# Performance work log

Measured on AMD Instinct MI355X. Metric: run time of the kernel, lower is better.

Reference implementation:

```python
import jax, jax.numpy as jnp
import numpy as np

B = 64          # batches
T = 65536       # total packed tokens
X = 512         # token feature dim
K = 5           # io pairs
Y = X * K       # extra dim = 2560
H = 512         # hidden


def setup_inputs() -> dict:
    key = jax.random.key(0)
    ks = jax.random.split(key, 13)
    s = 0.02  # weight scale
    return {
        "ps_data": jax.random.normal(ks[0], (T, X), jnp.float32),
        "io_embed": jax.random.normal(ks[1], (B, K, X), jnp.float32),
        "segment_ids": jnp.sort(jax.random.randint(ks[2], (T,), 0, B, dtype=jnp.int32)),
        # attention_fc: Linear(X+Y,512) -> ReLU -> Linear(512,512) -> ReLU -> Linear(512,1)
        "W1": jax.random.normal(ks[3], (X + Y, H), jnp.float32) * s,
        "b1": jnp.zeros((H,), jnp.float32),
        "W2": jax.random.normal(ks[4], (H, H), jnp.float32) * s,
        "b2": jnp.zeros((H,), jnp.float32),
        "W3": jax.random.normal(ks[5], (H, 1), jnp.float32) * s,
        "b3": jnp.zeros((1,), jnp.float32),
        # final_fc: Linear(512,512) -> ReLU -> Linear(512,2)
        "Wf1": jax.random.normal(ks[6], (H, H), jnp.float32) * s,
        "bf1": jnp.zeros((H,), jnp.float32),
        "Wf2": jax.random.normal(ks[7], (H, 2), jnp.float32) * s,
        "bf2": jnp.zeros((2,), jnp.float32),
    }


def reference(ps_data, io_embed, segment_ids, W1, b1, W2, b2, W3, b3, Wf1, bf1, Wf2, bf2):
    # io_embed (B,K,X) -> (B,Y); gather per token by its batch index
    extra = io_embed.reshape(B, -1)[segment_ids]            # (T, Y)
    h = jnp.concatenate([ps_data, extra], axis=1)           # (T, X+Y)
    h = jax.nn.relu(h @ W1 + b1)
    h = jax.nn.relu(h @ W2 + b2)
    logits = (h @ W3 + b3)[:, 0]                            # (T,)
    # per-segment softmax over ragged segments
    m = jax.lax.stop_gradient(
        jax.ops.segment_max(logits, segment_ids, num_segments=B))
    e = jnp.exp(logits - m[segment_ids])
    denom = jax.ops.segment_sum(e, segment_ids, num_segments=B)
    w = e / denom[segment_ids]                              # (T,)
    pooled = jax.ops.segment_sum(w[:, None] * ps_data, segment_ids,
                                 num_segments=B)            # (B, X)
    # final_fc
    return jax.nn.relu(pooled @ Wf1 + bf1) @ Wf2 + bf2      # (B, 2)
```

## Files before the change

### kernel.cpp

```cpp
#include <hip/hip_runtime.h>

#define T_TOK 65536
#define BATCH 64
#define XDIM  512
#define HDIM  512
#define YDIM  2560

#define BK 64
#define GM_TM 256
#define GM_TN 128

#define SB_KC 64
#define SB_KS 40
#define SB_BG 8

#define PREP_CONV   16384
#define PREP_TRANS  2048
#define PREP_SB     320

typedef float  f32x4  __attribute__((ext_vector_type(4)));
typedef __bf16 bf16x8 __attribute__((ext_vector_type(8)));

__device__ __forceinline__ unsigned short f2bf(float f) {
    unsigned int u = __float_as_uint(f);
    return (unsigned short)((u + 0x7FFFu + ((u >> 16) & 1u)) >> 16);
}

__device__ __forceinline__ float bf2f(unsigned short u) {
    return __uint_as_float((unsigned int)u << 16);
}

__device__ __forceinline__ void load_lds16(const unsigned short* g, unsigned short* l) {
    __builtin_amdgcn_global_load_lds(
        (const __attribute__((address_space(1))) unsigned int*)g,
        (__attribute__((address_space(3))) unsigned int*)l, 16, 0, 0);
}

__device__ __forceinline__ int lower_bound_seg(const int* __restrict__ s, int n, int v) {
    int lo = 0, hi = n;
    while (lo < hi) { int mid = (lo + hi) >> 1; if (s[mid] < v) lo = mid + 1; else hi = mid; }
    return lo;
}

__global__ __launch_bounds__(256) void prep_kernel(const float* __restrict__ ps,
                                                   unsigned short* __restrict__ psb,
                                                   const float* __restrict__ W1,
                                                   const float* __restrict__ W2,
                                                   unsigned short* __restrict__ w1t,
                                                   unsigned short* __restrict__ w2t,
                                                   const float* __restrict__ io,
                                                   float* __restrict__ partial) {
    __shared__ float sio[SB_BG][SB_KC];
    const int blk = blockIdx.x;
    const int t = threadIdx.x;

    if (blk < PREP_CONV) {
        size_t idx = (size_t)blk * 256 + t;
        const float4* s4 = reinterpret_cast<const float4*>(ps) + idx * 2;
        float4 a = s4[0], b = s4[1];
        ushort4 o0, o1;
        o0.x = f2bf(a.x); o0.y = f2bf(a.y); o0.z = f2bf(a.z); o0.w = f2bf(a.w);
        o1.x = f2bf(b.x); o1.y = f2bf(b.y); o1.z = f2bf(b.z); o1.w = f2bf(b.w);
        reinterpret_cast<ushort4*>(psb)[idx * 2 + 0] = o0;
        reinterpret_cast<ushort4*>(psb)[idx * 2 + 1] = o1;
    } else if (blk < PREP_CONV + PREP_TRANS) {
        int bb = blk - PREP_CONV;
        const float* src = bb < 1024 ? W1 : W2;
        unsigned short* dst = bb < 1024 ? w1t : w2t;
        int idx = (bb & 1023) * 256 + t;
        int nn = idx >> 9, kk = idx & 511;
        dst[idx] = f2bf(src[(size_t)kk * 512 + nn]);
    } else {
        int sb = blk - PREP_CONV - PREP_TRANS;
        int s = sb >> 3, g = sb & 7;
        for (int i = t; i < SB_BG * SB_KC; i += 256) {
            int bb = i >> 6, kk = i & 63;
            sio[bb][kk] = io[(size_t)(g * SB_BG + bb) * YDIM + s * SB_KC + kk];
        }
        __syncthreads();
        float acc[SB_BG][2] = {};
        const int k0 = 512 + s * SB_KC;
        #pragma unroll 4
        for (int kk = 0; kk < SB_KC; kk++) {
            float wa = W1[(size_t)(k0 + kk) * 512 + t];
            float wb = W1[(size_t)(k0 + kk) * 512 + t + 256];
            #pragma unroll
            for (int bb = 0; bb < SB_BG; bb++) {
                acc[bb][0] += sio[bb][kk] * wa;
                acc[bb][1] += sio[bb][kk] * wb;
            }
        }
        #pragma unroll
        for (int bb = 0; bb < SB_BG; bb++) {
            int b = g * SB_BG + bb;
            partial[((size_t)s * BATCH + b) * 512 + t]       = acc[bb][0];
            partial[((size_t)s * BATCH + b) * 512 + t + 256] = acc[bb][1];
        }
    }
}

__global__ __launch_bounds__(256) void segbias_reduce(const float* __restrict__ partial,
                                                      float* __restrict__ segbias) {
    int idx = blockIdx.x * 256 + threadIdx.x;
    float s = 0.f;
    #pragma unroll
    for (int i = 0; i < SB_KS; i++) s += partial[(size_t)i * BATCH * 512 + idx];
    segbias[idx] = s;
}

#define FRAG_AT(sh, R, c) (*reinterpret_cast<const bf16x8*>(&(sh)[((R) * 8 + (((c) ^ ((R) & 7)))) * 8]))

__global__ __launch_bounds__(512) void gemm1_kernel(const unsigned short* __restrict__ psb,
                                                    const unsigned short* __restrict__ w1t,
                                                    const float* __restrict__ segbias,
                                                    const float* __restrict__ b1,
                                                    const int* __restrict__ segids,
                                                    unsigned short* __restrict__ h1) {
    __shared__ unsigned short shA[GM_TM * BK];
    __shared__ unsigned short shB[GM_TN * BK];

    const int bid = blockIdx.x;
    const int xcd = bid & 7;
    const int j = bid >> 3;
    const int n0 = (j & 3) * GM_TN;
    const int m0 = ((j >> 2) * 8 + xcd) * GM_TM;
    const int t = threadIdx.x;
    const int w = t >> 6, L = t & 63;
    const int mbase = (w >> 1) * 64, nbase = (w & 1) * 64;
    const int lrow = L & 15, lq = L >> 4;

    f32x4 acc[4][4] = {};

    for (int kt = 0; kt < XDIM; kt += BK) {
        #pragma unroll
        for (int i_ = 0; i_ < 4; i_++) {
            int g_ = i_ * 512 + t;
            int r_ = g_ >> 3, c_ = g_ & 7, cs_ = c_ ^ (r_ & 7);
            load_lds16(psb + (size_t)(m0 + r_) * XDIM + kt + cs_ * 8, &shA[g_ * 8]);
        }
        #pragma unroll
        for (int i_ = 0; i_ < 2; i_++) {
            int g_ = i_ * 512 + t;
            int r_ = g_ >> 3, c_ = g_ & 7, cs_ = c_ ^ (r_ & 7);
            load_lds16(w1t + (size_t)(n0 + r_) * HDIM + kt + cs_ * 8, &shB[g_ * 8]);
        }
        __syncthreads();
        #pragma unroll
        for (int ks = 0; ks < BK; ks += 32) {
            bf16x8 af[4], bfr[4];
            #pragma unroll
            for (int i = 0; i < 4; i++) af[i] = FRAG_AT(shA, mbase + i * 16 + lrow, (ks >> 3) + lq);
            #pragma unroll
            for (int jj = 0; jj < 4; jj++) bfr[jj] = FRAG_AT(shB, nbase + jj * 16 + lrow, (ks >> 3) + lq);
            #pragma unroll
            for (int i = 0; i < 4; i++)
                #pragma unroll
                for (int jj = 0; jj < 4; jj++)
                    acc[i][jj] = __builtin_amdgcn_mfma_f32_16x16x32_bf16(af[i], bfr[jj], acc[i][jj], 0, 0, 0);
        }
        __syncthreads();
    }

    #pragma unroll
    for (int i = 0; i < 4; i++) {
        #pragma unroll
        for (int r = 0; r < 4; r++) {
            int gm = m0 + mbase + i * 16 + lq * 4 + r;
            int sg = segids[gm];
            const float* sb = segbias + (size_t)sg * HDIM;
            #pragma unroll
            for (int jj = 0; jj < 4; jj++) {
                int gn = n0 + nbase + jj * 16 + lrow;
                float v = acc[i][jj][r] + sb[gn] + b1[gn];
                v = v > 0.f ? v : 0.f;
                h1[(size_t)gm * HDIM + gn] = f2bf(v);
            }
        }
    }
}

__global__ __launch_bounds__(512) void gemm2_kernel(const unsigned short* __restrict__ h1,
                                                    const unsigned short* __restrict__ w2t,
                                                    const float* __restrict__ b2,
                                                    const float* __restrict__ w3,
                                                    float* __restrict__ logits8) {
    __shared__ unsigned short shA[GM_TM * BK];
    __shared__ unsigned short shB[GM_TN * BK];

    const int bid = blockIdx.x;
    const int xcd = bid & 7;
    const int j = bid >> 3;
    const int n0 = (j & 3) * GM_TN;
    const int m0 = ((j >> 2) * 8 + xcd) * GM_TM;
    const int t = threadIdx.x;
    const int w = t >> 6, L = t & 63;
    const int mbase = (w >> 1) * 64, nbase = (w & 1) * 64;
    const int lrow = L & 15, lq = L >> 4;

    f32x4 acc[4][4] = {};

    for (int kt = 0; kt < HDIM; kt += BK) {
        #pragma unroll
        for (int i_ = 0; i_ < 4; i_++) {
            int g_ = i_ * 512 + t;
            int r_ = g_ >> 3, c_ = g_ & 7, cs_ = c_ ^ (r_ & 7);
            load_lds16(h1 + (size_t)(m0 + r_) * HDIM + kt + cs_ * 8, &shA[g_ * 8]);
        }
        #pragma unroll
        for (int i_ = 0; i_ < 2; i_++) {
            int g_ = i_ * 512 + t;
            int r_ = g_ >> 3, c_ = g_ & 7, cs_ = c_ ^ (r_ & 7);
            load_lds16(w2t + (size_t)(n0 + r_) * HDIM + kt + cs_ * 8, &shB[g_ * 8]);
        }
        __syncthreads();
        #pragma unroll
        for (int ks = 0; ks < BK; ks += 32) {
            bf16x8 af[4], bfr[4];
            #pragma unroll
            for (int i = 0; i < 4; i++) af[i] = FRAG_AT(shA, mbase + i * 16 + lrow, (ks >> 3) + lq);
            #pragma unroll
            for (int jj = 0; jj < 4; jj++) bfr[jj] = FRAG_AT(shB, nbase + jj * 16 + lrow, (ks >> 3) + lq);
            #pragma unroll
            for (int i = 0; i < 4; i++)
                #pragma unroll
                for (int jj = 0; jj < 4; jj++)
                    acc[i][jj] = __builtin_amdgcn_mfma_f32_16x16x32_bf16(af[i], bfr[jj], acc[i][jj], 0, 0, 0);
        }
        __syncthreads();
    }

    float w3v[4], b2v[4];
    #pragma unroll
    for (int jj = 0; jj < 4; jj++) {
        int gn = n0 + nbase + jj * 16 + lrow;
        w3v[jj] = w3[gn];
        b2v[jj] = b2[gn];
    }
    const int slice = (j & 3) * 2 + (w & 1);
    #pragma unroll
    for (int i = 0; i < 4; i++) {
        #pragma unroll
        for (int r = 0; r < 4; r++) {
            float p = 0.f;
            #pragma unroll
            for (int jj = 0; jj < 4; jj++) {
                float h2 = acc[i][jj][r] + b2v[jj];
                h2 = h2 > 0.f ? h2 : 0.f;
                p += h2 * w3v[jj];
            }
            p += __shfl_xor(p, 1, 64);
            p += __shfl_xor(p, 2, 64);
            p += __shfl_xor(p, 4, 64);
            p += __shfl_xor(p, 8, 64);
            if (lrow == 0)
                logits8[(size_t)slice * T_TOK + m0 + mbase + i * 16 + lq * 4 + r] = p;
        }
    }
}

__global__ __launch_bounds__(256) void stats_kernel(const float* __restrict__ logits8,
                                                    float* __restrict__ logits,
                                                    const int* __restrict__ segids,
                                                    float* __restrict__ stats) {
    const int b = blockIdx.x;
    const int t = threadIdx.x;
    __shared__ float sred[4];
    const int start = lower_bound_seg(segids, T_TOK, b);
    const int end   = lower_bound_seg(segids, T_TOK, b + 1);
    float m = -3.4e38f;
    for (int i = start + t; i < end; i += 256) {
        float l = 0.f;
        #pragma unroll
        for (int s = 0; s < 8; s++) l += logits8[(size_t)s * T_TOK + i];
        logits[i] = l;
        m = fmaxf(m, l);
    }
    for (int d = 32; d; d >>= 1) m = fmaxf(m, __shfl_down(m, d, 64));
    if ((t & 63) == 0) sred[t >> 6] = m;
    __syncthreads();
    m = fmaxf(fmaxf(sred[0], sred[1]), fmaxf(sred[2], sred[3]));
    __syncthreads();
    float s = 0.f;
    for (int i = start + t; i < end; i += 256) s += __expf(logits[i] - m);
    for (int d = 32; d; d >>= 1) s += __shfl_down(s, d, 64);
    if ((t & 63) == 0) sred[t >> 6] = s;
    __syncthreads();
    if (t == 0) { stats[2 * b] = m; stats[2 * b + 1] = sred[0] + sred[1] + sred[2] + sred[3]; }
}

__global__ __launch_bounds__(512) void pool_kernel(const unsigned short* __restrict__ psb,
                                                   const float* __restrict__ logits,
                                                   const int* __restrict__ segids,
                                                   const float* __restrict__ stats,
                                                   float* __restrict__ pooled) {
    const int s = blockIdx.x;
    const int b = blockIdx.y;
    const int t = threadIdx.x;
    __shared__ float wv[512];
    const int start = lower_bound_seg(segids, T_TOK, b);
    const int end   = lower_bound_seg(segids, T_TOK, b + 1);
    const int n = end - start;
    const int per = (n + 15) >> 4;
    const int s0 = start + s * per;
    const int s1 = min(s0 + per, end);
    const float m = stats[2 * b];
    const float inv = 1.f / stats[2 * b + 1];
    float acc = 0.f;
    for (int base = s0; base < s1; base += 512) {
        int cnt = min(512, s1 - base);
        __syncthreads();
        if (t < cnt) wv[t] = __expf(logits[base + t] - m) * inv;
        __syncthreads();
        for (int i = 0; i < cnt; i++)
            acc += wv[i] * bf2f(psb[(size_t)(base + i) * XDIM + t]);
    }
    if (s1 > s0) atomicAdd(&pooled[b * XDIM + t], acc);
}

__global__ __launch_bounds__(512) void final_kernel(const float* __restrict__ pooled,
                                                    const float* __restrict__ wf1,
                                                    const float* __restrict__ bf1,
                                                    const float* __restrict__ wf2,
                                                    const float* __restrict__ bf2,
                                                    float* __restrict__ out) {
    const int b = blockIdx.x;
    const int t = threadIdx.x;
    __shared__ float sp[512];
    __shared__ float r0s[8], r1s[8];
    sp[t] = pooled[b * XDIM + t];
    __syncthreads();
    float acc = bf1[t];
    #pragma unroll 4
    for (int k = 0; k < 512; k++) acc += sp[k] * wf1[(size_t)k * 512 + t];
    float h = fmaxf(acc, 0.f);
    float p0 = h * wf2[t * 2 + 0];
    float p1 = h * wf2[t * 2 + 1];
    for (int d = 32; d; d >>= 1) { p0 += __shfl_down(p0, d, 64); p1 += __shfl_down(p1, d, 64); }
    if ((t & 63) == 0) { r0s[t >> 6] = p0; r1s[t >> 6] = p1; }
    __syncthreads();
    if (t == 0) {
        float a = 0.f, c = 0.f;
        #pragma unroll
        for (int i = 0; i < 8; i++) { a += r0s[i]; c += r1s[i]; }
        out[b * 2 + 0] = a + bf2[0];
        out[b * 2 + 1] = c + bf2[1];
    }
}

extern "C" void kernel_launch(void* const* d_in, const int* in_sizes, int n_in,
                              void* d_out, int out_size, void* d_ws, size_t ws_size,
                              hipStream_t stream) {
    const float* ps  = (const float*)d_in[0];
    const float* io  = (const float*)d_in[1];
    const int*   seg = (const int*)d_in[2];
    const float* W1  = (const float*)d_in[3];
    const float* b1  = (const float*)d_in[4];
    const float* W2  = (const float*)d_in[5];
    const float* b2  = (const float*)d_in[6];
    const float* W3  = (const float*)d_in[7];
    const float* Wf1 = (const float*)d_in[9];
    const float* bf1 = (const float*)d_in[10];
    const float* Wf2 = (const float*)d_in[11];
    const float* bf2 = (const float*)d_in[12];
    float* out = (float*)d_out;

    char* ws = (char*)d_ws;
    float*          segbias = (float*)(ws + 0);
    float*          logits  = (float*)(ws + 131072);
    float*          stats   = (float*)(ws + 393216);
    float*          pooled  = (float*)(ws + 397312);
    unsigned short* w1t     = (unsigned short*)(ws + 528384);
    unsigned short* w2t     = (unsigned short*)(ws + 1052672);
    float*          logits8 = (float*)(ws + 1576960);
    float*          partial = (float*)(ws + 3674112);
    unsigned short* psb     = (unsigned short*)(ws + 16777216);
    unsigned short* h1      = (unsigned short*)(ws + 83886080);

    hipMemsetAsync(ws + 397312, 0, 131072, stream);

    prep_kernel<<<PREP_CONV + PREP_TRANS + PREP_SB, 256, 0, stream>>>(
        ps, psb, W1, W2, w1t, w2t, io, partial);
    segbias_reduce<<<128, 256, 0, stream>>>(partial, segbias);
    gemm1_kernel<<<(T_TOK / GM_TM) * 4, 512, 0, stream>>>(psb, w1t, segbias, b1, seg, h1);
    gemm2_kernel<<<(T_TOK / GM_TM) * 4, 512, 0, stream>>>(h1, w2t, b2, W3, logits8);
    stats_kernel<<<64, 256, 0, stream>>>(logits8, logits, seg, stats);
    pool_kernel<<<dim3(16, 64), 512, 0, stream>>>(psb, logits, seg, stats, pooled);
    final_kernel<<<64, 512, 0, stream>>>(pooled, Wf1, bf1, Wf2, bf2, out);
}
```

Measured before the change: 391.7 us.

## Use 32x32 MFMA tiles in GEMMs and fuse softmax stats into pooling

Both GEMM kernels switch from 16x16x32 MFMA to 32x32x16 MFMA with 2x2 accumulator tiles per wave, cutting LDS fragment reads per MFMA, and the epilogues are remapped to the 32x32 output layout. The separate stats kernel is removed: each pool block recomputes the segment max and sum from the eight logit slices. Atomic pooling plus its memset are replaced by per-slice partial buffers that final_kernel sums. This drops two launches and the atomics, but every pool block redundantly reads the segment's logits, about 16x duplicated stats work.

New measurement: 398.4 us. Within noise of the previous version (+1.7%).

```diff
diff --git a/kernel.cpp b/kernel.cpp
--- a/kernel.cpp
+++ b/kernel.cpp
@@ -18,7 +18,7 @@
 #define PREP_TRANS  2048
 #define PREP_SB     320
 
-typedef float  f32x4  __attribute__((ext_vector_type(4)));
+typedef float  f32x16 __attribute__((ext_vector_type(16)));
 typedef __bf16 bf16x8 __attribute__((ext_vector_type(8)));
 
 __device__ __forceinline__ unsigned short f2bf(float f) {
@@ -127,9 +127,9 @@
     const int t = threadIdx.x;
     const int w = t >> 6, L = t & 63;
     const int mbase = (w >> 1) * 64, nbase = (w & 1) * 64;
-    const int lrow = L & 15, lq = L >> 4;
-
-    f32x4 acc[4][4] = {};
+    const int l31 = L & 31, lh = L >> 5;
+
+    f32x16 acc[2][2] = {};
 
     for (int kt = 0; kt < XDIM; kt += BK) {
         #pragma unroll
@@ -146,32 +146,36 @@
         }
         __syncthreads();
         #pragma unroll
-        for (int ks = 0; ks < BK; ks += 32) {
-            bf16x8 af[4], bfr[4];
-            #pragma unroll
-            for (int i = 0; i < 4; i++) af[i] = FRAG_AT(shA, mbase + i * 16 + lrow, (ks >> 3) + lq);
-            #pragma unroll
-            for (int jj = 0; jj < 4; jj++) bfr[jj] = FRAG_AT(shB, nbase + jj * 16 + lrow, (ks >> 3) + lq);
-            #pragma unroll
-            for (int i = 0; i < 4; i++)
+        for (int ks = 0; ks < 4; ks++) {
+            const int c = ks * 2 + lh;
+            bf16x8 af[2], bfr[2];
+            #pragma unroll
+            for (int i = 0; i < 2; i++)  af[i]  = FRAG_AT(shA, mbase + i * 32 + l31, c);
+            #pragma unroll
+            for (int jj = 0; jj < 2; jj++) bfr[jj] = FRAG_AT(shB, nbase + jj * 32 + l31, c);
+            #pragma unroll
+            for (int i = 0; i < 2; i++)
                 #pragma unroll
-                for (int jj = 0; jj < 4; jj++)
-                    acc[i][jj] = __builtin_amdgcn_mfma_f32_16x16x32_bf16(af[i], bfr[jj], acc[i][jj], 0, 0, 0);
-        }
-        __syncthreads();
-    }
-
-    #pragma unroll
-    for (int i = 0; i < 4; i++) {
-        #pragma unroll
-        for (int r = 0; r < 4; r++) {
-            int gm = m0 + mbase + i * 16 + lq * 4 + r;
+                for (int jj = 0; jj < 2; jj++)
+                    acc[i][jj] = __builtin_amdgcn_mfma_f32_32x32x16_bf16(af[i], bfr[jj], acc[i][jj], 0, 0, 0);
+        }
+        __syncthreads();
+    }
+
+    float b1v[2];
+    #pragma unroll
+    for (int jj = 0; jj < 2; jj++) b1v[jj] = b1[n0 + nbase + jj * 32 + l31];
+    #pragma unroll
+    for (int i = 0; i < 2; i++) {
+        #pragma unroll
+        for (int r = 0; r < 16; r++) {
+            int gm = m0 + mbase + i * 32 + (r & 3) + 8 * (r >> 2) + 4 * lh;
             int sg = segids[gm];
             const float* sb = segbias + (size_t)sg * HDIM;
             #pragma unroll
-            for (int jj = 0; jj < 4; jj++) {
-                int gn = n0 + nbase + jj * 16 + lrow;
-                float v = acc[i][jj][r] + sb[gn] + b1[gn];
+            for (int jj = 0; jj < 2; jj++) {
+                int gn = n0 + nbase + jj * 32 + l31;
+                float v = acc[i][jj][r] + sb[gn] + b1v[jj];
                 v = v > 0.f ? v : 0.f;
                 h1[(size_t)gm * HDIM + gn] = f2bf(v);
             }
@@ -195,9 +199,9 @@
     const int t = threadIdx.x;
     const int w = t >> 6, L = t & 63;
     const int mbase = (w >> 1) * 64, nbase = (w & 1) * 64;
-    const int lrow = L & 15, lq = L >> 4;
-
-    f32x4 acc[4][4] = {};
+    const int l31 = L & 31, lh = L >> 5;
+
+    f32x16 acc[2][2] = {};
 
     for (int kt = 0; kt < HDIM; kt += BK) {
         #pragma unroll
@@ -214,36 +218,37 @@
         }
         __syncthreads();
         #pragma unroll
-        for (int ks = 0; ks < BK; ks += 32) {
-            bf16x8 af[4], bfr[4];
-            #pragma unroll
-            for (int i = 0; i < 4; i++) af[i] = FRAG_AT(shA, mbase + i * 16 + lrow, (ks >> 3) + lq);
-            #pragma unroll
-            for (int jj = 0; jj < 4; jj++) bfr[jj] = FRAG_AT(shB, nbase + jj * 16 + lrow, (ks >> 3) + lq);
-            #pragma unroll
-            for (int i = 0; i < 4; i++)
+        for (int ks = 0; ks < 4; ks++) {
+            const int c = ks * 2 + lh;
+            bf16x8 af[2], bfr[2];
+            #pragma unroll
+            for (int i = 0; i < 2; i++)  af[i]  = FRAG_AT(shA, mbase + i * 32 + l31, c);
+            #pragma unroll
+            for (int jj = 0; jj < 2; jj++) bfr[jj] = FRAG_AT(shB, nbase + jj * 32 + l31, c);
+            #pragma unroll
+            for (int i = 0; i < 2; i++)
                 #pragma unroll
-                for (int jj = 0; jj < 4; jj++)
-                    acc[i][jj] = __builtin_amdgcn_mfma_f32_16x16x32_bf16(af[i], bfr[jj], acc[i][jj], 0, 0, 0);
-        }
-        __syncthreads();
-    }
-
-    float w3v[4], b2v[4];
-    #pragma unroll
-    for (int jj = 0; jj < 4; jj++) {
-        int gn = n0 + nbase + jj * 16 + lrow;
+                for (int jj = 0; jj < 2; jj++)
+                    acc[i][jj] = __builtin_amdgcn_mfma_f32_32x32x16_bf16(af[i], bfr[jj], acc[i][jj], 0, 0, 0);
+        }
+        __syncthreads();
+    }
+
+    float w3v[2], b2v[2];
+    #pragma unroll
+    for (int jj = 0; jj < 2; jj++) {
+        int gn = n0 + nbase + jj * 32 + l31;
         w3v[jj] = w3[gn];
         b2v[jj] = b2[gn];
     }
     const int slice = (j & 3) * 2 + (w & 1);
     #pragma unroll
-    for (int i = 0; i < 4; i++) {
-        #pragma unroll
-        for (int r = 0; r < 4; r++) {
+    for (int i = 0; i < 2; i++) {
+        #pragma unroll
+        for (int r = 0; r < 16; r++) {
             float p = 0.f;
             #pragma unroll
-            for (int jj = 0; jj < 4; jj++) {
+            for (int jj = 0; jj < 2; jj++) {
                 float h2 = acc[i][jj][r] + b2v[jj];
                 h2 = h2 > 0.f ? h2 : 0.f;
                 p += h2 * w3v[jj];
@@ -252,72 +257,77 @@
             p += __shfl_xor(p, 2, 64);
             p += __shfl_xor(p, 4, 64);
             p += __shfl_xor(p, 8, 64);
-            if (lrow == 0)
-                logits8[(size_t)slice * T_TOK + m0 + mbase + i * 16 + lq * 4 + r] = p;
-        }
-    }
-}
-
-__global__ __launch_bounds__(256) void stats_kernel(const float* __restrict__ logits8,
-                                                    float* __restrict__ logits,
-                                                    const int* __restrict__ segids,
-                                                    float* __restrict__ stats) {
-    const int b = blockIdx.x;
-    const int t = threadIdx.x;
-    __shared__ float sred[4];
+            p += __shfl_xor(p, 16, 64);
+            if (l31 == 0)
+                logits8[(size_t)slice * T_TOK + m0 + mbase + i * 32 +
+                        (r & 3) + 8 * (r >> 2) + 4 * lh] = p;
+        }
+    }
+}
+
+__global__ __launch_bounds__(512) void pool_kernel(const unsigned short* __restrict__ psb,
+                                                   const float* __restrict__ logits8,
+                                                   const int* __restrict__ segids,
+                                                   float* __restrict__ pooled16) {
+    const int s = blockIdx.x;
+    const int b = blockIdx.y;
+    const int t = threadIdx.x;
+    __shared__ float wv[512];
+    __shared__ float sred[8];
     const int start = lower_bound_seg(segids, T_TOK, b);
     const int end   = lower_bound_seg(segids, T_TOK, b + 1);
+
     float m = -3.4e38f;
-    for (int i = start + t; i < end; i += 256) {
+    for (int i = start + t; i < end; i += 512) {
         float l = 0.f;
         #pragma unroll
-        for (int s = 0; s < 8; s++) l += logits8[(size_t)s * T_TOK + i];
-        logits[i] = l;
+        for (int k = 0; k < 8; k++) l += logits8[(size_t)k * T_TOK + i];
         m = fmaxf(m, l);
     }
     for (int d = 32; d; d >>= 1) m = fmaxf(m, __shfl_down(m, d, 64));
     if ((t & 63) == 0) sred[t >> 6] = m;
     __syncthreads();
-    m = fmaxf(fmaxf(sred[0], sred[1]), fmaxf(sred[2], sred[3]));
-    __syncthreads();
-    float s = 0.f;
-    for (int i = start + t; i < end; i += 256) s += __expf(logits[i] - m);
-    for (int d = 32; d; d >>= 1) s += __shfl_down(s, d, 64);
-    if ((t & 63) == 0) sred[t >> 6] = s;
-    __syncthreads();
-    if (t == 0) { stats[2 * b] = m; stats[2 * b + 1] = sred[0] + sred[1] + sred[2] + sred[3]; }
-}
-
-__global__ __launch_bounds__(512) void pool_kernel(const unsigned short* __restrict__ psb,
-                                                   const float* __restrict__ logits,
-                                                   const int* __restrict__ segids,
-                                                   const float* __restrict__ stats,
-                                                   float* __restrict__ pooled) {
-    const int s = blockIdx.x;
-    const int b = blockIdx.y;
-    const int t = threadIdx.x;
-    __shared__ float wv[512];
-    const int start = lower_bound_seg(segids, T_TOK, b);
-    const int end   = lower_bound_seg(segids, T_TOK, b + 1);
+    m = sred[0];
+    #pragma unroll
+    for (int k = 1; k < 8; k++) m = fmaxf(m, sred[k]);
+    __syncthreads();
+    float ss = 0.f;
+    for (int i = start + t; i < end; i += 512) {
+        float l = 0.f;
+        #pragma unroll
+        for (int k = 0; k < 8; k++) l += logits8[(size_t)k * T_TOK + i];
+        ss += __expf(l - m);
+    }
+    for (int d = 32; d; d >>= 1) ss += __shfl_down(ss, d, 64);
+    if ((t & 63) == 0) sred[t >> 6] = ss;
+    __syncthreads();
+    float denom = 0.f;
+    #pragma unroll
+    for (int k = 0; k < 8; k++) denom += sred[k];
+    const float inv = 1.f / denom;
+
     const int n = end - start;
     const int per = (n + 15) >> 4;
     const int s0 = start + s * per;
     const int s1 = min(s0 + per, end);
-    const float m = stats[2 * b];
-    const float inv = 1.f / stats[2 * b + 1];
     float acc = 0.f;
     for (int base = s0; base < s1; base += 512) {
         int cnt = min(512, s1 - base);
         __syncthreads();
-        if (t < cnt) wv[t] = __expf(logits[base + t] - m) * inv;
+        if (t < cnt) {
+            float l = 0.f;
+            #pragma unroll
+            for (int k = 0; k < 8; k++) l += logits8[(size_t)k * T_TOK + base + t];
+            wv[t] = __expf(l - m) * inv;
+        }
         __syncthreads();
         for (int i = 0; i < cnt; i++)
             acc += wv[i] * bf2f(psb[(size_t)(base + i) * XDIM + t]);
     }
-    if (s1 > s0) atomicAdd(&pooled[b * XDIM + t], acc);
-}
-
-__global__ __launch_bounds__(512) void final_kernel(const float* __restrict__ pooled,
+    pooled16[((size_t)s * BATCH + b) * XDIM + t] = acc;
+}
+
+__global__ __launch_bounds__(512) void final_kernel(const float* __restrict__ pooled16,
                                                     const float* __restrict__ wf1,
                                                     const float* __restrict__ bf1,
                                                     const float* __restrict__ wf2,
@@ -327,7 +337,10 @@
     const int t = threadIdx.x;
     __shared__ float sp[512];
     __shared__ float r0s[8], r1s[8];
-    sp[t] = pooled[b * XDIM + t];
+    float pv = 0.f;
+    #pragma unroll
+    for (int k = 0; k < 16; k++) pv += pooled16[((size_t)k * BATCH + b) * XDIM + t];
+    sp[t] = pv;
     __syncthreads();
     float acc = bf1[t];
     #pragma unroll 4
@@ -365,25 +378,20 @@
     float* out = (float*)d_out;
 
     char* ws = (char*)d_ws;
-    float*          segbias = (float*)(ws + 0);
-    float*          logits  = (float*)(ws + 131072);
-    float*          stats   = (float*)(ws + 393216);
-    float*          pooled  = (float*)(ws + 397312);
-    unsigned short* w1t     = (unsigned short*)(ws + 528384);
-    unsigned short* w2t     = (unsigned short*)(ws + 1052672);
-    float*          logits8 = (float*)(ws + 1576960);
-    float*          partial = (float*)(ws + 3674112);
-    unsigned short* psb     = (unsigned short*)(ws + 16777216);
-    unsigned short* h1      = (unsigned short*)(ws + 83886080);
-
-    hipMemsetAsync(ws + 397312, 0, 131072, stream);
+    float*          segbias  = (float*)(ws + 0);
+    unsigned short* w1t      = (unsigned short*)(ws + 131072);
+    unsigned short* w2t      = (unsigned short*)(ws + 655360);
+    float*          logits8  = (float*)(ws + 1179648);
+    float*          pooled16 = (float*)(ws + 3276800);
+    float*          partial  = (float*)(ws + 5373952);
+    unsigned short* psb      = (unsigned short*)(ws + 16777216);
+    unsigned short* h1       = (unsigned short*)(ws + 83886080);
 
     prep_kernel<<<PREP_CONV + PREP_TRANS + PREP_SB, 256, 0, stream>>>(
         ps, psb, W1, W2, w1t, w2t, io, partial);
     segbias_reduce<<<128, 256, 0, stream>>>(partial, segbias);
     gemm1_kernel<<<(T_TOK / GM_TM) * 4, 512, 0, stream>>>(psb, w1t, segbias, b1, seg, h1);
     gemm2_kernel<<<(T_TOK / GM_TM) * 4, 512, 0, stream>>>(h1, w2t, b2, W3, logits8);
-    stats_kernel<<<64, 256, 0, stream>>>(logits8, logits, seg, stats);
-    pool_kernel<<<dim3(16, 64), 512, 0, stream>>>(psb, logits, seg, stats, pooled);
-    final_kernel<<<64, 512, 0, stream>>>(pooled, Wf1, bf1, Wf2, bf2, out);
-}
+    pool_kernel<<<dim3(16, 64), 512, 0, stream>>>(psb, logits8, seg, pooled16);
+    final_kernel<<<64, 512, 0, stream>>>(pooled16, Wf1, bf1, Wf2, bf2, out);
+}
```
